# Performance work log

Hardware: AMD Instinct MI355X
Metric: run time of the kernel (lower is better)

The kernel has to match this reference:

```python
import jax, jax.numpy as jnp
import numpy as np

# SOM hyperparameters (match init_kwargs)
M, N_GRID = 32, 32
D = 512
BATCH = 8192
ALPHA = 0.5          # learning_rate
NUM_EPOCH_BP = 5     # hard-coded in call(): self.backprop(self.count, 5)
ITER = 0             # first call: count == 0
RADIUS_FACTOR = 1.1
GAUSSIAN_STD = 0.08
SIGMA = max(M, N_GRID) * RADIUS_FACTOR  # 35.2


def setup_inputs() -> dict:
    key = jax.random.key(0)
    k1, k2 = jax.random.split(key)
    x = jax.random.normal(k1, (BATCH, D), dtype=jnp.float32)
    som_map = jax.random.uniform(k2, (M * N_GRID, D), dtype=jnp.float32)  # RandomUniform(0,1)
    ii, jj = np.meshgrid(np.arange(M), np.arange(N_GRID), indexing='ij')
    locs = jnp.asarray(np.stack([ii.ravel(), jj.ravel()], axis=1), dtype=jnp.int32)  # [N,2]
    return {"x": x, "som_map": som_map, "locs": locs}


def reference(x, som_map, locs):
    # --- feedforward: BMU search ---
    # squared_distance[b,n] = ||x[b] - map[n]||^2, computed without the [B,N,D] blowup
    x2 = jnp.sum(x * x, axis=1, keepdims=True)                 # [B,1]
    m2 = jnp.sum(som_map * som_map, axis=1)[None, :]           # [1,N]
    sqd = x2 + m2 - 2.0 * (x @ som_map.T)                      # [B,N]
    bmu_indices = jnp.argmin(sqd, axis=1)                      # [B]
    bmu_locs = locs[bmu_indices]                               # [B,2] int

    # --- backprop (iter=0, num_epoch=5) ---
    decay = ITER * (ALPHA - 1.0) / (NUM_EPOCH_BP - 1.0)
    radius = SIGMA - decay
    alpha = ALPHA - decay

    # bmu_distance_squares[b,n] = ||locs[n] - bmu_locs[b]||^2 (grid coords)
    diff = locs[None, :, :] - bmu_locs[:, None, :]             # [B,N,2] small (int)
    bmu_d2 = jnp.sum(diff * diff, axis=2).astype(jnp.float32)  # [B,N]
    impact = jnp.exp(-bmu_d2 / (2.0 * (radius * GAUSSIAN_STD) ** 2))  # [B,N]
    lr = impact * alpha                                        # [B,N]

    # weight_update[n,d] = sum_b lr[b,n] * (x[b,d] - map[n,d])
    # = einsum('bn,bd->nd') - map * sum_b lr   (avoids the [B,N,D] intermediate)
    weight_update = jnp.einsum('bn,bd->nd', lr, x) - som_map * jnp.sum(lr, axis=0)[:, None]
    return som_map + weight_update
```

## Files before the change

### kernel.cpp

```cpp
#include <hip/hip_runtime.h>
#include <stdint.h>

#define D 512
#define KTOT 1024
#define BATCH 8192
#define NMAP 1024
#define GRID_W 32
#define ALPHA 0.5f
#define C2 15.859712f

typedef __attribute__((ext_vector_type(4))) float f32x4;
typedef __attribute__((ext_vector_type(8))) short bf16x8;
typedef __attribute__((ext_vector_type(8))) unsigned short u16x8;

static __device__ __forceinline__ unsigned short f2bf(float f) {
    uint32_t u = __float_as_uint(f);
    uint32_t r = (u + 0x7FFFu + ((u >> 16) & 1u)) >> 16;
    return (unsigned short)r;
}
static __device__ __forceinline__ float bf2f(unsigned short h) {
    return __uint_as_float(((uint32_t)h) << 16);
}

__global__ __launch_bounds__(256) void k_prep(const float* __restrict__ x,
                                              const float* __restrict__ map,
                                              unsigned short* __restrict__ As,
                                              unsigned short* __restrict__ Bs,
                                              float* __restrict__ m2,
                                              unsigned long long* __restrict__ packed) {
    int bid = blockIdx.x;
    if (bid < BATCH * (D / 8) / 256) {
        int g = bid * 256 + threadIdx.x;
        if (g < BATCH) packed[g] = 0xFFFFFFFFFFFFFFFFull;
        int b = g >> 6;
        int k8 = (g & 63) << 3;
        const float* xp = x + (size_t)b * D + k8;
        float4 v0 = *(const float4*)xp;
        float4 v1 = *(const float4*)(xp + 4);
        float vv[8] = {v0.x, v0.y, v0.z, v0.w, v1.x, v1.y, v1.z, v1.w};
        u16x8 hi, lo;
        #pragma unroll
        for (int j = 0; j < 8; j++) {
            unsigned short h = f2bf(vv[j]);
            hi[j] = h;
            lo[j] = f2bf(vv[j] - bf2f(h));
        }
        unsigned short* row = As + (size_t)b * KTOT;
        *(u16x8*)(row + k8) = hi;
        *(u16x8*)(row + 512 + k8) = lo;
    } else {
        int mb = bid - BATCH * (D / 8) / 256;
        int n = mb * 4 + (threadIdx.x >> 6);
        int lane = threadIdx.x & 63;
        const float* mp = map + (size_t)n * D + lane * 8;
        float4 v0 = *(const float4*)mp;
        float4 v1 = *(const float4*)(mp + 4);
        float vv[8] = {v0.x, v0.y, v0.z, v0.w, v1.x, v1.y, v1.z, v1.w};
        u16x8 hi;
        float s = 0.f;
        #pragma unroll
        for (int j = 0; j < 8; j++) {
            s += vv[j] * vv[j];
            hi[j] = f2bf(vv[j]);
        }
        *(u16x8*)(Bs + (size_t)n * 512 + lane * 8) = hi;
        #pragma unroll
        for (int off = 32; off > 0; off >>= 1) s += __shfl_down(s, off);
        if (lane == 0) m2[n] = s;
    }
}

#define BM 128
#define BN 64
#define BK 64

__global__ __launch_bounds__(256) void k_bmu(const unsigned short* __restrict__ As,
                                             const unsigned short* __restrict__ Bs,
                                             const float* __restrict__ m2,
                                             unsigned long long* __restrict__ packed) {
    __shared__ unsigned short Al[BM * BK];
    __shared__ unsigned short Bl[BN * BK];
    const int xcd = blockIdx.x & 7;
    const int j = blockIdx.x >> 3;
    const int b0 = (xcd * 8 + (j & 7)) * BM;
    const int n0 = (j >> 3) * BN;
    const int t = threadIdx.x;
    const int w = t >> 6, l = t & 63;
    const int wm = w >> 1, wn = w & 1;

    f32x4 acc[4][2];
    #pragma unroll
    for (int i = 0; i < 4; i++)
        #pragma unroll
        for (int jj = 0; jj < 2; jj++) acc[i][jj] = (f32x4)(0.f);

    const int srow = l >> 3;
    const int sslot = (l & 7) ^ (l >> 3);
    const unsigned short* agp0 = As + (size_t)(b0 + w * 32 + srow) * KTOT + sslot * 8;
    const unsigned short* bgp0 = Bs + (size_t)(n0 + w * 16 + srow) * 512 + sslot * 8;

    for (int kt = 0; kt < KTOT; kt += BK) {
        int ktb = kt & 511;
        #pragma unroll
        for (int i = 0; i < 4; i++) {
            __builtin_amdgcn_global_load_lds(
                (const __attribute__((address_space(1))) void*)(agp0 + (size_t)i * 8 * KTOT + kt),
                (__attribute__((address_space(3))) void*)(Al + w * 2048 + i * 512), 16, 0, 0);
        }
        #pragma unroll
        for (int i = 0; i < 2; i++) {
            __builtin_amdgcn_global_load_lds(
                (const __attribute__((address_space(1))) void*)(bgp0 + (size_t)i * 8 * 512 + ktb),
                (__attribute__((address_space(3))) void*)(Bl + w * 1024 + i * 512), 16, 0, 0);
        }
        __syncthreads();

        #pragma unroll
        for (int kk = 0; kk < 2; kk++) {
            bf16x8 af[4], bfr[2];
            #pragma unroll
            for (int mi = 0; mi < 4; mi++) {
                int r = wm * 64 + mi * 16 + (l & 15);
                int slot = kk * 4 + (l >> 4);
                af[mi] = *(const bf16x8*)&Al[r * 64 + ((slot ^ (r & 7)) << 3)];
            }
            #pragma unroll
            for (int nj = 0; nj < 2; nj++) {
                int r = wn * 32 + nj * 16 + (l & 15);
                int slot = kk * 4 + (l >> 4);
                bfr[nj] = *(const bf16x8*)&Bl[r * 64 + ((slot ^ (r & 7)) << 3)];
            }
            #pragma unroll
            for (int mi = 0; mi < 4; mi++)
                #pragma unroll
                for (int nj = 0; nj < 2; nj++)
                    acc[mi][nj] = __builtin_amdgcn_mfma_f32_16x16x32_bf16(
                        af[mi], bfr[nj], acc[mi][nj], 0, 0, 0);
        }
        __syncthreads();
    }

    float m2v[2];
    #pragma unroll
    for (int nj = 0; nj < 2; nj++)
        m2v[nj] = m2[n0 + wn * 32 + nj * 16 + (l & 15)];

    #pragma unroll
    for (int mi = 0; mi < 4; mi++) {
        #pragma unroll
        for (int reg = 0; reg < 4; reg++) {
            float best = m2v[0] - 2.0f * acc[mi][0][reg];
            int bi = n0 + wn * 32 + (l & 15);
            {
                float v = m2v[1] - 2.0f * acc[mi][1][reg];
                int n = n0 + wn * 32 + 16 + (l & 15);
                if (v < best) { best = v; bi = n; }
            }
            #pragma unroll
            for (int msk = 1; msk <= 8; msk <<= 1) {
                float ov = __shfl_xor(best, msk);
                int oi = __shfl_xor(bi, msk);
                if (ov < best || (ov == best && oi < bi)) { best = ov; bi = oi; }
            }
            if ((l & 15) == 0) {
                unsigned int fb = __float_as_uint(best);
                fb = (fb & 0x80000000u) ? ~fb : (fb | 0x80000000u);
                unsigned long long key =
                    ((unsigned long long)fb << 32) | (unsigned int)bi;
                int row = b0 + wm * 64 + mi * 16 + (l >> 4) * 4 + reg;
                atomicMin(&packed[row], key);
            }
        }
    }
}

__global__ __launch_bounds__(256) void k_scatter(const float* __restrict__ x,
                                                 const unsigned long long* __restrict__ packed,
                                                 float* __restrict__ S,
                                                 int* __restrict__ cnt) {
    __shared__ int list[BATCH];
    __shared__ int cnts[256];
    __shared__ int offs[256];
    int g = blockIdx.x;
    int t = threadIdx.x;
    int b0 = t * (BATCH / 256);

    int mybmu[BATCH / 256];
    int c = 0;
    #pragma unroll
    for (int i = 0; i < BATCH / 256; i++) {
        mybmu[i] = (int)(packed[b0 + i] & 0xFFFFFFFFull);
        c += (mybmu[i] == g) ? 1 : 0;
    }
    cnts[t] = c;
    offs[t] = c;
    __syncthreads();
    #pragma unroll
    for (int s = 1; s < 256; s <<= 1) {
        int v = (t >= s) ? offs[t - s] : 0;
        __syncthreads();
        offs[t] += v;
        __syncthreads();
    }
    int off = offs[t] - cnts[t];
    #pragma unroll
    for (int i = 0; i < BATCH / 256; i++) {
        if (mybmu[i] == g) list[off++] = b0 + i;
    }
    __syncthreads();
    int len = offs[255];

    float acc0 = 0.f, acc1 = 0.f;
    for (int i = 0; i < len; i++) {
        const float* xr = x + (size_t)list[i] * D;
        acc0 += xr[t];
        acc1 += xr[t + 256];
    }
    S[(size_t)g * D + t] = acc0;
    S[(size_t)g * D + t + 256] = acc1;
    if (t == 0) cnt[g] = len;
}

__global__ __launch_bounds__(256) void k_conv1(const float* __restrict__ S,
                                               float* __restrict__ V,
                                               const int* __restrict__ cnt,
                                               float* __restrict__ sum_lr) {
    __shared__ float tbl[GRID_W];
    __shared__ float vc[GRID_W][GRID_W];
    int gi = blockIdx.x;
    int d = blockIdx.y * 256 + threadIdx.x;
    if (threadIdx.x < GRID_W)
        tbl[threadIdx.x] = __expf(-(float)(threadIdx.x * threadIdx.x) / C2);
    __syncthreads();
    float acc[GRID_W];
    #pragma unroll
    for (int nj = 0; nj < GRID_W; nj++) acc[nj] = 0.f;
    for (int gj = 0; gj < GRID_W; gj++) {
        float s = S[(size_t)(gi * GRID_W + gj) * D + d];
        #pragma unroll
        for (int nj = 0; nj < GRID_W; nj++) {
            int dd = nj - gj; dd = dd < 0 ? -dd : dd;
            acc[nj] += tbl[dd] * s;
        }
    }
    #pragma unroll
    for (int nj = 0; nj < GRID_W; nj++)
        V[(size_t)(gi * GRID_W + nj) * D + d] = acc[nj];

    if (blockIdx.x == 0 && blockIdx.y == 0) {
        int t = threadIdx.x;
        #pragma unroll
        for (int j = 0; j < 4; j++) {
            int idx = t * 4 + j;
            int a = idx >> 5, b = idx & 31;
            float s = 0.f;
            for (int gj = 0; gj < GRID_W; gj++) {
                int dd = gj - b; dd = dd < 0 ? -dd : dd;
                s += tbl[dd] * (float)cnt[a * GRID_W + gj];
            }
            vc[a][b] = s;
        }
        __syncthreads();
        #pragma unroll
        for (int j = 0; j < 4; j++) {
            int idx = t * 4 + j;
            int a = idx >> 5, b = idx & 31;
            float s2 = 0.f;
            for (int gg = 0; gg < GRID_W; gg++) {
                int dd = gg - a; dd = dd < 0 ? -dd : dd;
                s2 += tbl[dd] * vc[gg][b];
            }
            sum_lr[idx] = ALPHA * s2;
        }
    }
}

__global__ __launch_bounds__(256) void k_conv2(const float* __restrict__ V,
                                               const float* __restrict__ map,
                                               const float* __restrict__ sum_lr,
                                               float* __restrict__ out) {
    __shared__ float tbl[GRID_W];
    int nj = blockIdx.x;
    int d = blockIdx.y * 256 + threadIdx.x;
    if (threadIdx.x < GRID_W)
        tbl[threadIdx.x] = __expf(-(float)(threadIdx.x * threadIdx.x) / C2);
    __syncthreads();
    float acc[GRID_W];
    #pragma unroll
    for (int ni = 0; ni < GRID_W; ni++) acc[ni] = 0.f;
    for (int gi = 0; gi < GRID_W; gi++) {
        float v = V[(size_t)(gi * GRID_W + nj) * D + d];
        #pragma unroll
        for (int ni = 0; ni < GRID_W; ni++) {
            int dd = ni - gi; dd = dd < 0 ? -dd : dd;
            acc[ni] += tbl[dd] * v;
        }
    }
    #pragma unroll
    for (int ni = 0; ni < GRID_W; ni++) {
        int n = ni * GRID_W + nj;
        out[(size_t)n * D + d] =
            map[(size_t)n * D + d] * (1.0f - sum_lr[n]) + ALPHA * acc[ni];
    }
}

extern "C" void kernel_launch(void* const* d_in, const int* in_sizes, int n_in,
                              void* d_out, int out_size, void* d_ws, size_t ws_size,
                              hipStream_t stream) {
    (void)in_sizes; (void)n_in; (void)out_size; (void)ws_size;
    const float* x = (const float*)d_in[0];
    const float* map = (const float*)d_in[1];
    float* out = (float*)d_out;

    char* ws = (char*)d_ws;
    unsigned long long* packed = (unsigned long long*)(ws);
    float* m2 = (float*)(ws + 65536);
    int* cnt = (int*)(ws + 69632);
    float* sum_lr = (float*)(ws + 73728);
    float* S = (float*)(ws + 77824);
    float* V = (float*)(ws + 2174976);
    unsigned short* As = (unsigned short*)(ws + 4272128);
    unsigned short* Bs = (unsigned short*)(ws + 21049344);

    k_prep<<<BATCH * (D / 8) / 256 + NMAP / 4, 256, 0, stream>>>(x, map, As, Bs, m2, packed);
    k_bmu<<<(BATCH / BM) * (NMAP / BN), 256, 0, stream>>>(As, Bs, m2, packed);
    k_scatter<<<NMAP, 256, 0, stream>>>(x, packed, S, cnt);
    k_conv1<<<dim3(GRID_W, D / 256), 256, 0, stream>>>(S, V, cnt, sum_lr);
    k_conv2<<<dim3(GRID_W, D / 256), 256, 0, stream>>>(V, map, sum_lr, out);
}
```

Measured before the change: 98.39 us.

## Fuse separable Gaussian convolution passes into one LDS-tiled kernel

Merges the two separable neighbourhood-convolution kernels into a single kernel. Each block loads an 8-column slice of S for all 1024 map nodes into LDS, does both 1-D passes in registers and LDS, and recomputes sum_lr per block, so the V intermediate and the extra launch go away. The scatter accumulation loop is also unrolled by two with independent accumulators to expose more memory-level parallelism. In exchange the grid drops to 64 blocks with large LDS use, and every block redundantly recomputes the count convolution.

```diff
diff --git a/kernel.cpp b/kernel.cpp
--- a/kernel.cpp
+++ b/kernel.cpp
@@ -8,6 +8,7 @@
 #define GRID_W 32
 #define ALPHA 0.5f
 #define C2 15.859712f
+#define DC 8
 
 typedef __attribute__((ext_vector_type(4))) float f32x4;
 typedef __attribute__((ext_vector_type(8))) short bf16x8;
@@ -210,97 +211,82 @@
     __syncthreads();
     int len = offs[255];
 
-    float acc0 = 0.f, acc1 = 0.f;
-    for (int i = 0; i < len; i++) {
+    float a0 = 0.f, a1 = 0.f, c0 = 0.f, c1 = 0.f;
+    int i = 0;
+    for (; i + 2 <= len; i += 2) {
+        const float* xr0 = x + (size_t)list[i] * D;
+        const float* xr1 = x + (size_t)list[i + 1] * D;
+        a0 += xr0[t]; a1 += xr0[t + 256];
+        c0 += xr1[t]; c1 += xr1[t + 256];
+    }
+    if (i < len) {
         const float* xr = x + (size_t)list[i] * D;
-        acc0 += xr[t];
-        acc1 += xr[t + 256];
-    }
-    S[(size_t)g * D + t] = acc0;
-    S[(size_t)g * D + t + 256] = acc1;
+        a0 += xr[t]; a1 += xr[t + 256];
+    }
+    S[(size_t)g * D + t] = a0 + c0;
+    S[(size_t)g * D + t + 256] = a1 + c1;
     if (t == 0) cnt[g] = len;
 }
 
-__global__ __launch_bounds__(256) void k_conv1(const float* __restrict__ S,
-                                               float* __restrict__ V,
-                                               const int* __restrict__ cnt,
-                                               float* __restrict__ sum_lr) {
+__global__ __launch_bounds__(256) void k_conv(const float* __restrict__ S,
+                                              const int* __restrict__ cnt,
+                                              const float* __restrict__ map,
+                                              float* __restrict__ out) {
+    __shared__ float T[NMAP][DC + 1];
     __shared__ float tbl[GRID_W];
-    __shared__ float vc[GRID_W][GRID_W];
-    int gi = blockIdx.x;
-    int d = blockIdx.y * 256 + threadIdx.x;
-    if (threadIdx.x < GRID_W)
-        tbl[threadIdx.x] = __expf(-(float)(threadIdx.x * threadIdx.x) / C2);
+    __shared__ float vcB[GRID_W][GRID_W];
+    int t = threadIdx.x;
+    int d0 = blockIdx.x * DC;
+    if (t < GRID_W) tbl[t] = __expf(-(float)(t * t) / C2);
+    #pragma unroll
+    for (int p = 0; p < 8; p++) {
+        int idx = p * 256 + t;
+        int row = idx >> 1, half = (idx & 1) * 4;
+        float4 v = *(const float4*)(S + (size_t)row * D + d0 + half);
+        T[row][half + 0] = v.x; T[row][half + 1] = v.y;
+        T[row][half + 2] = v.z; T[row][half + 3] = v.w;
+    }
     __syncthreads();
-    float acc[GRID_W];
-    #pragma unroll
-    for (int nj = 0; nj < GRID_W; nj++) acc[nj] = 0.f;
-    for (int gj = 0; gj < GRID_W; gj++) {
-        float s = S[(size_t)(gi * GRID_W + gj) * D + d];
-        #pragma unroll
-        for (int nj = 0; nj < GRID_W; nj++) {
+    #pragma unroll
+    for (int jj = 0; jj < 4; jj++) {
+        int idx = t * 4 + jj;
+        int a = idx >> 5, b = idx & 31;
+        float s = 0.f;
+        for (int gj = 0; gj < GRID_W; gj++) {
+            int dd = gj - b; dd = dd < 0 ? -dd : dd;
+            s += tbl[dd] * (float)cnt[a * GRID_W + gj];
+        }
+        vcB[a][b] = s;
+    }
+    __syncthreads();
+
+    int nj = (t >> 3) & 31;
+    int dc = t & 7;
+    float vreg[GRID_W];
+    #pragma unroll
+    for (int gi = 0; gi < GRID_W; gi++) {
+        float s = 0.f;
+        #pragma unroll
+        for (int gj = 0; gj < GRID_W; gj++) {
             int dd = nj - gj; dd = dd < 0 ? -dd : dd;
-            acc[nj] += tbl[dd] * s;
-        }
-    }
-    #pragma unroll
-    for (int nj = 0; nj < GRID_W; nj++)
-        V[(size_t)(gi * GRID_W + nj) * D + d] = acc[nj];
-
-    if (blockIdx.x == 0 && blockIdx.y == 0) {
-        int t = threadIdx.x;
-        #pragma unroll
-        for (int j = 0; j < 4; j++) {
-            int idx = t * 4 + j;
-            int a = idx >> 5, b = idx & 31;
-            float s = 0.f;
-            for (int gj = 0; gj < GRID_W; gj++) {
-                int dd = gj - b; dd = dd < 0 ? -dd : dd;
-                s += tbl[dd] * (float)cnt[a * GRID_W + gj];
-            }
-            vc[a][b] = s;
-        }
-        __syncthreads();
-        #pragma unroll
-        for (int j = 0; j < 4; j++) {
-            int idx = t * 4 + j;
-            int a = idx >> 5, b = idx & 31;
-            float s2 = 0.f;
-            for (int gg = 0; gg < GRID_W; gg++) {
-                int dd = gg - a; dd = dd < 0 ? -dd : dd;
-                s2 += tbl[dd] * vc[gg][b];
-            }
-            sum_lr[idx] = ALPHA * s2;
-        }
-    }
-}
-
-__global__ __launch_bounds__(256) void k_conv2(const float* __restrict__ V,
-                                               const float* __restrict__ map,
-                                               const float* __restrict__ sum_lr,
-                                               float* __restrict__ out) {
-    __shared__ float tbl[GRID_W];
-    int nj = blockIdx.x;
-    int d = blockIdx.y * 256 + threadIdx.x;
-    if (threadIdx.x < GRID_W)
-        tbl[threadIdx.x] = __expf(-(float)(threadIdx.x * threadIdx.x) / C2);
-    __syncthreads();
-    float acc[GRID_W];
-    #pragma unroll
-    for (int ni = 0; ni < GRID_W; ni++) acc[ni] = 0.f;
-    for (int gi = 0; gi < GRID_W; gi++) {
-        float v = V[(size_t)(gi * GRID_W + nj) * D + d];
-        #pragma unroll
-        for (int ni = 0; ni < GRID_W; ni++) {
+            s += tbl[dd] * T[gi * GRID_W + gj][dc];
+        }
+        vreg[gi] = s;
+    }
+    #pragma unroll
+    for (int ni = 0; ni < GRID_W; ni++) {
+        float u = 0.f;
+        float s2 = 0.f;
+        #pragma unroll
+        for (int gi = 0; gi < GRID_W; gi++) {
             int dd = ni - gi; dd = dd < 0 ? -dd : dd;
-            acc[ni] += tbl[dd] * v;
-        }
-    }
-    #pragma unroll
-    for (int ni = 0; ni < GRID_W; ni++) {
+            u += tbl[dd] * vreg[gi];
+            s2 += tbl[dd] * vcB[gi][nj];
+        }
+        float slr = ALPHA * s2;
         int n = ni * GRID_W + nj;
-        out[(size_t)n * D + d] =
-            map[(size_t)n * D + d] * (1.0f - sum_lr[n]) + ALPHA * acc[ni];
+        out[(size_t)n * D + d0 + dc] =
+            map[(size_t)n * D + d0 + dc] * (1.0f - slr) + ALPHA * u;
     }
 }
 
@@ -316,15 +302,12 @@
     unsigned long long* packed = (unsigned long long*)(ws);
     float* m2 = (float*)(ws + 65536);
     int* cnt = (int*)(ws + 69632);
-    float* sum_lr = (float*)(ws + 73728);
-    float* S = (float*)(ws + 77824);
-    float* V = (float*)(ws + 2174976);
-    unsigned short* As = (unsigned short*)(ws + 4272128);
-    unsigned short* Bs = (unsigned short*)(ws + 21049344);
+    float* S = (float*)(ws + 73728);
+    unsigned short* As = (unsigned short*)(ws + 2170880);
+    unsigned short* Bs = (unsigned short*)(ws + 18948096);
 
     k_prep<<<BATCH * (D / 8) / 256 + NMAP / 4, 256, 0, stream>>>(x, map, As, Bs, m2, packed);
     k_bmu<<<(BATCH / BM) * (NMAP / BN), 256, 0, stream>>>(As, Bs, m2, packed);
     k_scatter<<<NMAP, 256, 0, stream>>>(x, packed, S, cnt);
-    k_conv1<<<dim3(GRID_W, D / 256), 256, 0, stream>>>(S, V, cnt, sum_lr);
-    k_conv2<<<dim3(GRID_W, D / 256), 256, 0, stream>>>(V, map, sum_lr, out);
-}
+    k_conv<<<D / DC, 256, 0, stream>>>(S, cnt, map, out);
+}
```

After: 97.66 us. No clear change (-0.7%).
